# Kernel tuning notes

Hardware: AMD Instinct MI355X
Metric: run time of the kernel (lower is better)

## Reference

```python
import jax, jax.numpy as jnp
import numpy as np

ROI_SIZE = 14      # pooled output HxW
BASE_SIZE = 28
SR = 2             # bilinear sampling ratio per bin (torchvision default -1 is adaptive;
                   # a fixed ratio of 2 is the standard Mask R-CNN setting and keeps shapes static)


def _prep_coord(c, L):
    """torchvision bilinear index/weight prep along one axis. c: [R,G] sample coords."""
    valid = (c >= -1.0) & (c <= L)            # points outside [-1, L] contribute 0
    c = jnp.clip(c, 0.0, L - 1)
    lo = jnp.floor(c)
    frac = c - lo
    lo_i = lo.astype(jnp.int32)
    hi_i = lo_i + 1
    at_edge = lo_i >= L - 1
    lo_i = jnp.where(at_edge, L - 1, lo_i)
    hi_i = jnp.where(at_edge, L - 1, hi_i)
    frac = jnp.where(at_edge, 0.0, frac)
    return lo_i, hi_i, frac, valid


def roi_align(feat, boxes, out=ROI_SIZE, sr=SR):
    """feat: [1,C,H,W]; boxes: [R,4] (x1,y1,x2,y2) in feature coords. Returns [R,C,out,out].
    Matches torchvision ops.roi_align(spatial_scale=1, aligned=False) with sampling_ratio=sr."""
    f = feat[0]
    C, H, W = f.shape
    ff = f.reshape(C, H * W)
    x1, y1, x2, y2 = boxes[:, 0], boxes[:, 1], boxes[:, 2], boxes[:, 3]
    roi_w = jnp.maximum(x2 - x1, 1.0)
    roi_h = jnp.maximum(y2 - y1, 1.0)
    G = out * sr
    steps = (jnp.arange(G, dtype=boxes.dtype) + 0.5) / sr  # in units of one bin
    ys = y1[:, None] + steps[None, :] * (roi_h / out)[:, None]  # [R,G]
    xs = x1[:, None] + steps[None, :] * (roi_w / out)[:, None]  # [R,G]

    yl, yh, fy, vy = _prep_coord(ys, H)
    xl, xh, fx, vx = _prep_coord(xs, W)
    mask = (vy[:, :, None] & vx[:, None, :]).astype(f.dtype)   # [R,G,G]
    wll = (1.0 - fy)[:, :, None] * (1.0 - fx)[:, None, :] * mask
    wlh = (1.0 - fy)[:, :, None] * fx[:, None, :] * mask
    whl = fy[:, :, None] * (1.0 - fx)[:, None, :] * mask
    whh = fy[:, :, None] * fx[:, None, :] * mask

    def gath(yi, xi):
        idx = yi[:, :, None] * W + xi[:, None, :]  # [R,G,G] flat indices
        return ff[:, idx]                          # [C,R,G,G]

    v = (gath(yl, xl) * wll + gath(yl, xh) * wlh
         + gath(yh, xl) * whl + gath(yh, xh) * whh)   # [C,R,G,G]
    # average the sr x sr samples inside each output bin
    v = v.reshape(C, -1, out, sr, out, sr).mean(axis=(3, 5))  # [C,R,out,out]
    return jnp.transpose(v, (1, 0, 2, 3))


def setup_inputs() -> dict:
    key = jax.random.key(0)
    ks = jax.random.split(key, 6)
    feats = {}
    for j, hw in enumerate([224, 112, 56, 28]):
        feats[f"feat{j}"] = jax.random.normal(ks[j], (1, 256, hw, hw), dtype=jnp.float32)
    # normalized boxes in [0,1] with positive width/height: (x1, y1, x2, y2)
    tl = jax.random.uniform(ks[4], (512, 2), dtype=jnp.float32) * 0.6
    wh = jax.random.uniform(ks[5], (512, 2), dtype=jnp.float32) * 0.35 + 0.05
    rois = jnp.concatenate([tl, tl + wh], axis=1)
    feats["rois"] = rois
    return feats


def reference(feat0, feat1, feat2, feat3, rois):
    feats = [feat0, feat1, feat2, feat3]   # biggest (N2) ... smallest (N5)
    pooled = None
    r = rois
    # faithful to the source: `rois` is re-scaled cumulatively inside the loop
    for i in range(3, -1, -1):
        r = r * (2.0 ** i * BASE_SIZE)
        p = roi_align(feats[i], r)
        pooled = p if pooled is None else jnp.maximum(pooled, p)
    return pooled
```

## Files before the change

kernel.cpp:

```cpp
#include <hip/hip_runtime.h>

#define OUTS 14
#define GRIDG 28
#define NLEV 4
#define NPIX (OUTS*OUTS)
#define CG   32
#define NCG  8

typedef float floatx4 __attribute__((ext_vector_type(4)));

__global__ __launch_bounds__(256) void afp_kernel(
    const float* __restrict__ f0, const float* __restrict__ f1,
    const float* __restrict__ f2, const float* __restrict__ f3,
    const float* __restrict__ rois, float* __restrict__ out,
    int R, int C)
{
    __shared__ int    s_lo[2][NLEV][GRIDG];
    __shared__ int    s_hi[2][NLEV][GRIDG];
    __shared__ float  s_fr[2][NLEV][GRIDG];
    __shared__ int    s_va[2][NLEV][GRIDG];
    __shared__ int    s_lvact[NLEV];
    __shared__ int    s_nact;
    __shared__ int    s_plist[NPIX];
    __shared__ float2 s_tab[16][NPIX];

    const int bx  = blockIdx.x;
    const int r   = bx >> 3;
    const int cg  = bx & 7;
    const int tid = threadIdx.x;
    const int HS[NLEV] = {224, 112, 56, 28};
    const float* const fp[NLEV] = {f0, f1, f2, f3};
    const int cbase = cg * CG;

    {
        floatx4 z = {0.0f, 0.0f, 0.0f, 0.0f};
        floatx4* o4 = reinterpret_cast<floatx4*>(out + ((size_t)r * C + cbase) * NPIX);
        const int NQ = CG * NPIX / 4;
        for (int q = tid; q < NQ; q += 256)
            __builtin_nontemporal_store(z, o4 + q);
    }

    if (tid < 2 * NLEV * GRIDG) {
        int lv   = tid / (2 * GRIDG);
        int rem  = tid - lv * 2 * GRIDG;
        int axis = rem / GRIDG;
        int g    = rem - axis * GRIDG;

        float x1 = rois[4*r+0], y1 = rois[4*r+1];
        float x2 = rois[4*r+2], y2 = rois[4*r+3];
        for (int j = 3; j >= lv; --j) {
            float f = (float)(28 << j);
            x1 = __fmul_rn(x1, f); y1 = __fmul_rn(y1, f);
            x2 = __fmul_rn(x2, f); y2 = __fmul_rn(y2, f);
        }
        float lo_c = axis ? x1 : y1;
        float hi_c = axis ? x2 : y2;
        int   Li = HS[lv];
        float Lf = (float)Li;

        float span = fmaxf(__fsub_rn(hi_c, lo_c), 1.0f);
        float bin  = __fdiv_rn(span, (float)OUTS);
        float step = ((float)g + 0.5f) * 0.5f;
        float c    = __fadd_rn(lo_c, __fmul_rn(step, bin));

        int valid = (c >= -1.0f) && (c <= Lf);
        float cc  = fminf(fmaxf(c, 0.0f), Lf - 1.0f);
        float fl  = floorf(cc);
        float fr  = __fsub_rn(cc, fl);
        int lo = (int)fl, hi = lo + 1;
        if (lo >= Li - 1) { lo = Li - 1; hi = Li - 1; fr = 0.0f; }

        s_lo[axis][lv][g] = lo;  s_hi[axis][lv][g] = hi;
        s_fr[axis][lv][g] = fr;  s_va[axis][lv][g] = valid;
    } else if (tid < 2 * NLEV * GRIDG + NLEV) {
        s_lvact[tid - 2 * NLEV * GRIDG] = 0;
    } else if (tid == 2 * NLEV * GRIDG + NLEV) {
        s_nact = 0;
    }
    __syncthreads();

    if (tid < NPIX) {
        int oy = tid / OUTS, ox = tid - oy * OUTS;
        int gy = 2 * oy, gx = 2 * ox;
        int act = 0;
        #pragma unroll
        for (int lv = 0; lv < NLEV; ++lv) {
            int ay = s_va[0][lv][gy] | s_va[0][lv][gy+1];
            int ax = s_va[1][lv][gx] | s_va[1][lv][gx+1];
            if (ay & ax) { s_lvact[lv] = 1; act = 1; }
        }
        if (act) {
            int pos = atomicAdd(&s_nact, 1);
            s_plist[pos] = tid;
        }
    }
    __syncthreads();

    const int nact = s_nact;
    if (nact == 0) return;

    bool first = true;
    for (int lv = 0; lv < NLEV; ++lv) {
        if (!s_lvact[lv]) continue;

        if (tid < NPIX) {
            int oy = tid / OUTS, ox = tid - oy * OUTS;
            int gy = 2 * oy, gx = 2 * ox;
            int W = HS[lv];
            #pragma unroll
            for (int sy = 0; sy < 2; ++sy) {
                int   yv  = s_va[0][lv][gy+sy];
                int   ylo = s_lo[0][lv][gy+sy] * W;
                int   yhi = s_hi[0][lv][gy+sy] * W;
                float fy  = s_fr[0][lv][gy+sy];
                #pragma unroll
                for (int sx = 0; sx < 2; ++sx) {
                    int   xv  = s_va[1][lv][gx+sx];
                    int   xlo = s_lo[1][lv][gx+sx];
                    int   xhi = s_hi[1][lv][gx+sx];
                    float fx  = s_fr[1][lv][gx+sx];
                    float m   = (yv & xv) ? 1.0f : 0.0f;
                    int e = (sy * 2 + sx) * 4;
                    s_tab[e+0][tid] = make_float2(m*(1.0f-fy)*(1.0f-fx), __int_as_float(ylo+xlo));
                    s_tab[e+1][tid] = make_float2(m*(1.0f-fy)*fx,        __int_as_float(ylo+xhi));
                    s_tab[e+2][tid] = make_float2(m*fy*(1.0f-fx),        __int_as_float(yhi+xlo));
                    s_tab[e+3][tid] = make_float2(m*fy*fx,               __int_as_float(yhi+xhi));
                }
            }
        }
        __syncthreads();

        const int W = HS[lv];
        const int cl = tid >> 3;
        const int k  = tid & 7;
        const float* __restrict__ base = fp[lv] + (size_t)(cbase + cl) * W * W;
        for (int pi = k; pi < nact; pi += 8) {
            int p = s_plist[pi];
            float acc = 0.0f;
            #pragma unroll
            for (int e = 0; e < 16; ++e) {
                float2 t = s_tab[e][p];
                acc += t.x * base[__float_as_int(t.y)];
            }
            float val = acc * 0.25f;
            size_t off = ((size_t)r * C + cbase + cl) * NPIX + p;
            if (first) out[off] = fmaxf(val, 0.0f);
            else       out[off] = fmaxf(out[off], val);
        }
        __syncthreads();
        first = false;
    }
}

extern "C" void kernel_launch(void* const* d_in, const int* in_sizes, int n_in,
                              void* d_out, int out_size, void* d_ws, size_t ws_size,
                              hipStream_t stream) {
    const float* f0   = (const float*)d_in[0];
    const float* f1   = (const float*)d_in[1];
    const float* f2   = (const float*)d_in[2];
    const float* f3   = (const float*)d_in[3];
    const float* rois = (const float*)d_in[4];
    float* out = (float*)d_out;

    int R = in_sizes[4] / 4;
    int C = in_sizes[3] / (28 * 28);

    afp_kernel<<<R * NCG, 256, 0, stream>>>(f0, f1, f2, f3, rois, out, R, C);
}
```

Before: 153.2 us.

## Accumulate level maxima in registers and write float4 quads once

Active pixels are now grouped into quads of four, and each thread keeps per-quad running maxima in a register array across all pyramid levels. Outputs are written once with 16-byte nontemporal stores instead of being read and rewritten at every level. The up-front zero fill now covers only inactive quads, so most output bytes are no longer stored twice. The register array raises register pressure, and the wider quad granularity can do extra work on pixels inside a quad that are not active.

```diff
diff --git a/kernel.cpp b/kernel.cpp
--- a/kernel.cpp
+++ b/kernel.cpp
@@ -4,6 +4,7 @@
 #define GRIDG 28
 #define NLEV 4
 #define NPIX (OUTS*OUTS)
+#define NQ4  (NPIX/4)
 #define CG   32
 #define NCG  8
 
@@ -19,9 +20,10 @@
     __shared__ int    s_hi[2][NLEV][GRIDG];
     __shared__ float  s_fr[2][NLEV][GRIDG];
     __shared__ int    s_va[2][NLEV][GRIDG];
-    __shared__ int    s_lvact[NLEV];
-    __shared__ int    s_nact;
-    __shared__ int    s_plist[NPIX];
+    __shared__ int    s_axany[2][NLEV];
+    __shared__ int    s_qact[NQ4];
+    __shared__ int    s_qlist[NQ4];
+    __shared__ int    s_nq;
     __shared__ float2 s_tab[16][NPIX];
 
     const int bx  = blockIdx.x;
@@ -31,14 +33,6 @@
     const int HS[NLEV] = {224, 112, 56, 28};
     const float* const fp[NLEV] = {f0, f1, f2, f3};
     const int cbase = cg * CG;
-
-    {
-        floatx4 z = {0.0f, 0.0f, 0.0f, 0.0f};
-        floatx4* o4 = reinterpret_cast<floatx4*>(out + ((size_t)r * C + cbase) * NPIX);
-        const int NQ = CG * NPIX / 4;
-        for (int q = tid; q < NQ; q += 256)
-            __builtin_nontemporal_store(z, o4 + q);
-    }
 
     if (tid < 2 * NLEV * GRIDG) {
         int lv   = tid / (2 * GRIDG);
@@ -72,37 +66,58 @@
 
         s_lo[axis][lv][g] = lo;  s_hi[axis][lv][g] = hi;
         s_fr[axis][lv][g] = fr;  s_va[axis][lv][g] = valid;
-    } else if (tid < 2 * NLEV * GRIDG + NLEV) {
-        s_lvact[tid - 2 * NLEV * GRIDG] = 0;
-    } else if (tid == 2 * NLEV * GRIDG + NLEV) {
-        s_nact = 0;
+    } else if (tid == 2 * NLEV * GRIDG) {
+        s_nq = 0;
     }
     __syncthreads();
 
-    if (tid < NPIX) {
-        int oy = tid / OUTS, ox = tid - oy * OUTS;
-        int gy = 2 * oy, gx = 2 * ox;
+    if (tid < NQ4) {
         int act = 0;
         #pragma unroll
-        for (int lv = 0; lv < NLEV; ++lv) {
-            int ay = s_va[0][lv][gy] | s_va[0][lv][gy+1];
-            int ax = s_va[1][lv][gx] | s_va[1][lv][gx+1];
-            if (ay & ax) { s_lvact[lv] = 1; act = 1; }
+        for (int j = 0; j < 4; ++j) {
+            int p  = tid * 4 + j;
+            int oy = p / OUTS, ox = p - oy * OUTS;
+            int gy = 2 * oy, gx = 2 * ox;
+            #pragma unroll
+            for (int lv = 0; lv < NLEV; ++lv) {
+                int ay = s_va[0][lv][gy] | s_va[0][lv][gy+1];
+                int ax = s_va[1][lv][gx] | s_va[1][lv][gx+1];
+                act |= (ay & ax);
+            }
         }
-        if (act) {
-            int pos = atomicAdd(&s_nact, 1);
-            s_plist[pos] = tid;
-        }
+        s_qact[tid] = act;
+        if (act) s_qlist[atomicAdd(&s_nq, 1)] = tid;
+    } else if (tid >= 64 && tid < 64 + 2 * NLEV) {
+        int t = tid - 64, axis = t & 1, lv = t >> 1;
+        int any = 0;
+        #pragma unroll
+        for (int g = 0; g < GRIDG; ++g) any |= s_va[axis][lv][g];
+        s_axany[axis][lv] = any;
     }
     __syncthreads();
 
-    const int nact = s_nact;
-    if (nact == 0) return;
+    const int naq = s_nq;
 
-    bool first = true;
+    {
+        floatx4 z = {0.0f, 0.0f, 0.0f, 0.0f};
+        floatx4* o4 = reinterpret_cast<floatx4*>(out + ((size_t)r * C + cbase) * NPIX);
+        for (int i = tid; i < CG * NQ4; i += 256) {
+            int qq = i % NQ4;
+            if (!s_qact[qq]) __builtin_nontemporal_store(z, o4 + i);
+        }
+    }
+    if (naq == 0) return;
+
+    const int cl = tid >> 3;
+    const int k  = tid & 7;
+    floatx4 acc[7];
+    #pragma unroll
+    for (int t = 0; t < 7; ++t) acc[t] = (floatx4){0.f, 0.f, 0.f, 0.f};
+
     for (int lv = 0; lv < NLEV; ++lv) {
-        if (!s_lvact[lv]) continue;
+        if (!(s_axany[0][lv] & s_axany[1][lv])) continue;
 
+        __syncthreads();
         if (tid < NPIX) {
             int oy = tid / OUTS, ox = tid - oy * OUTS;
             int gy = 2 * oy, gx = 2 * ox;
@@ -131,24 +146,30 @@
         __syncthreads();
 
         const int W = HS[lv];
-        const int cl = tid >> 3;
-        const int k  = tid & 7;
         const float* __restrict__ base = fp[lv] + (size_t)(cbase + cl) * W * W;
-        for (int pi = k; pi < nact; pi += 8) {
-            int p = s_plist[pi];
-            float acc = 0.0f;
+        int t = 0;
+        for (int qi = k; qi < naq; qi += 8, ++t) {
+            int p0 = s_qlist[qi] * 4;
             #pragma unroll
-            for (int e = 0; e < 16; ++e) {
-                float2 t = s_tab[e][p];
-                acc += t.x * base[__float_as_int(t.y)];
+            for (int j = 0; j < 4; ++j) {
+                float v = 0.0f;
+                #pragma unroll
+                for (int e = 0; e < 16; ++e) {
+                    float2 tb = s_tab[e][p0 + j];
+                    v += tb.x * base[__float_as_int(tb.y)];
+                }
+                acc[t][j] = fmaxf(acc[t][j], v * 0.25f);
             }
-            float val = acc * 0.25f;
-            size_t off = ((size_t)r * C + cbase + cl) * NPIX + p;
-            if (first) out[off] = fmaxf(val, 0.0f);
-            else       out[off] = fmaxf(out[off], val);
         }
-        __syncthreads();
-        first = false;
+    }
+
+    {
+        floatx4* o4 = reinterpret_cast<floatx4*>(out + ((size_t)r * C + cbase) * NPIX);
+        int t = 0;
+        for (int qi = k; qi < naq; qi += 8, ++t) {
+            int q = s_qlist[qi];
+            __builtin_nontemporal_store(acc[t], o4 + cl * NQ4 + q);
+        }
     }
 }
 
```

Result: slower. 162.0 us (+5.8%).
